# Performance work log

Hardware: AMD Instinct MI355X
Metric: run time of the kernel (lower is better)

Reference implementation:

```python
import jax, jax.numpy as jnp
import numpy as np

N, P = 512, 256
GAMMA = 1.0


def _linear_w(key, out_dim, in_dim):
    # torch nn.Linear default init: U(-1/sqrt(fan_in), 1/sqrt(fan_in))
    bound = 1.0 / np.sqrt(in_dim)
    return jax.random.uniform(key, (out_dim, in_dim), jnp.float32, -bound, bound)


def setup_inputs() -> dict:
    key = jax.random.key(0)
    ks = jax.random.split(key, 11)
    grad = jax.random.normal(ks[0], (N, P), jnp.float32)
    gradm1 = jax.random.normal(ks[1], (N, P), jnp.float32)
    dm1 = jax.random.normal(ks[2], (N, P), jnp.float32)
    # reset_mat(n_traj=N): identity per trajectory
    predicted_mat = jnp.broadcast_to(jnp.eye(P, dtype=jnp.float32), (N, P, P)).copy()
    return {
        "grad": grad, "gradm1": gradm1, "dm1": dm1, "predicted_mat": predicted_mat,
        "W_fullskip": _linear_w(ks[3], 1, 6),
        "Wo1": _linear_w(ks[4], 6, 3),
        "Wo2": _linear_w(ks[5], 12, 6),
        "Wo3": _linear_w(ks[6], 3, 12),
        "Wl1": _linear_w(ks[7], 12, 6),
        "Wl2": _linear_w(ks[8], 24, 12),
        "Wl3": _linear_w(ks[9], 1, 24),
    }


def reference(grad, gradm1, dm1, predicted_mat, W_fullskip, Wo1, Wo2, Wo3, Wl1, Wl2, Wl3):
    relu = jax.nn.relu
    # --- construct_features (torch.no_grad) ---
    QNDG = jnp.einsum('npq,nq->np', predicted_mat, grad - gradm1)          # (N,P)
    Bg = -GAMMA * jnp.einsum('npq,nq->np', predicted_mat, grad)            # (N,P)
    # cat along feature dim then reshape(N,3,P).transpose -> stack on last axis
    x = jnp.stack([QNDG, dm1, Bg], axis=-1)                                # (N,P,3)
    x = jax.lax.stop_gradient(x)
    # --- outer_FF: per-coordinate tiny MLP, then mean over P ---
    of = relu(x @ Wo1.T)
    of = relu(of @ Wo2.T)
    of = of @ Wo3.T                                                        # (N,P,3)
    of = jnp.mean(of, axis=1)                                              # (N,3)
    of = jnp.broadcast_to(of[:, None, :], x.shape)                         # (N,P,3)
    x6 = jnp.concatenate([x, of], axis=-1)                                 # (N,P,6)
    # --- full skip connection ---
    fullskip = (x6 @ W_fullskip.T)[..., 0]                                 # (N,P)
    # --- inner MLP (layers) ---
    out = relu(x6 @ Wl1.T)
    out = relu(out @ Wl2.T)
    out = (out @ Wl3.T)[..., 0]                                            # (N,P)
    out = out + fullskip
    # --- BFGS-like rank-2 update ---
    DGK = grad - gradm1                                                    # (N,P)
    secant = x[:, :, 1] - x[:, :, 0]                                       # dm1 - QNDG
    denom = jnp.sum(out * DGK, axis=-1, keepdims=True)                     # (N,1)
    normalization = (1.0 / denom)[:, :, None]                              # (N,1,1)
    coef = (jnp.sum(secant * DGK, axis=-1, keepdims=True) / denom)[:, :, None]
    upd = normalization * (
        secant[:, :, None] * out[:, None, :]
        + out[:, :, None] * secant[:, None, :]
        - coef * out[:, :, None] * out[:, None, :]
    )                                                                      # (N,P,P)
    new_mat = predicted_mat + upd
    v = -jax.lax.stop_gradient(grad)
    d = jnp.einsum('npq,nq->np', new_mat, v)                               # (N,P)
    return d
```

## Files before the change

### kernel.cpp

```cpp
#include <hip/hip_runtime.h>

#define NT 512
#define PD 256
#define TROWS 32
#define NTILES 8
#define LPITCH 257

__device__ __forceinline__ float wave_reduce_sum(float v) {
    #pragma unroll
    for (int m = 32; m >= 1; m >>= 1) v += __shfl_xor(v, m, 64);
    return v;
}

__global__ __launch_bounds__(256) void fused_kernel(
    const float* __restrict__ pm, const float* __restrict__ grad,
    const float* __restrict__ gradm1, const float* __restrict__ dm1,
    const float* __restrict__ Wfs, const float* __restrict__ Wo1,
    const float* __restrict__ Wo2, const float* __restrict__ Wo3,
    const float* __restrict__ Wl1, const float* __restrict__ Wl2,
    const float* __restrict__ Wl3, float* __restrict__ dout)
{
    __shared__ float buf0[TROWS * LPITCH];
    __shared__ float buf1[TROWS * LPITCH];
    __shared__ float sW[516];
    __shared__ float redA[4][3];
    __shared__ float redB[4][4];

    const int t    = threadIdx.x;
    const int lane = t & 63;
    const int wave = t >> 6;
    const int n    = blockIdx.x;

    if (t < 18) sW[t]       = Wo1[t];
    if (t < 72) sW[18 + t]  = Wo2[t];
    if (t < 36) sW[90 + t]  = Wo3[t];
    if (t < 72) sW[126 + t] = Wl1[t];
    sW[198 + t] = Wl2[t];
    if (t < 32) sW[198 + 256 + t] = Wl2[256 + t];
    if (t < 24) sW[486 + t] = Wl3[t];
    if (t < 6)  sW[510 + t] = Wfs[t];

    const int r  = t & 31;
    const int cg = t >> 5;
    float gv[32], dgv[32];
    {
        const float4* gb  = (const float4*)(grad   + n * PD + cg * 32);
        const float4* gmb = (const float4*)(gradm1 + n * PD + cg * 32);
        #pragma unroll
        for (int i = 0; i < 8; ++i) {
            float4 a = gb[i];
            float4 b = gmb[i];
            gv[4*i+0] = a.x; gv[4*i+1] = a.y; gv[4*i+2] = a.z; gv[4*i+3] = a.w;
            dgv[4*i+0] = a.x - b.x; dgv[4*i+1] = a.y - b.y;
            dgv[4*i+2] = a.z - b.z; dgv[4*i+3] = a.w - b.w;
        }
    }

    const float* tbase = pm + (size_t)n * PD * PD;
    float4 stg[8];
    float accq[NTILES], accg[NTILES];


    #pragma unroll
    for (int j = 0; j < 8; ++j) {
        const int row = 4 * j + wave;
        stg[j] = ((const float4*)(tbase + (size_t)(0 * TROWS + row) * PD))[lane];
    }
    #pragma unroll
    for (int j = 0; j < 8; ++j) {
        const int row = 4 * j + wave;
        float* p = buf0 + row * LPITCH + lane;
        p[0] = stg[j].x; p[64] = stg[j].y; p[128] = stg[j].z; p[192] = stg[j].w;
    }
    __syncthreads();

    #pragma unroll
    for (int k = 0; k < NTILES; ++k) {
        if (k + 1 < NTILES) {
            #pragma unroll
            for (int j = 0; j < 8; ++j) {
                const int row = 4 * j + wave;
                stg[j] = ((const float4*)(tbase + (size_t)((k + 1) * TROWS + row) * PD))[lane];
            }
        }
        {
            const float* bp = ((k & 1) ? buf1 : buf0) + r * LPITCH + 8 * cg;
            float sq = 0.f, sg = 0.f;
            #pragma unroll
            for (int p = 0; p < 4; ++p) {
                #pragma unroll
                for (int q = 0; q < 8; ++q) {
                    const float m = bp[p * 64 + q];
                    sq += m * dgv[4*q + p];
                    sg += m * gv[4*q + p];
                }
            }
            accq[k] = sq; accg[k] = sg;
        }
        if (k + 1 < NTILES) {
            float* wb = ((k + 1) & 1) ? buf1 : buf0;
            #pragma unroll
            for (int j = 0; j < 8; ++j) {
                const int row = 4 * j + wave;
                float* p = wb + row * LPITCH + lane;
                p[0] = stg[j].x; p[64] = stg[j].y; p[128] = stg[j].z; p[192] = stg[j].w;
            }
        }
        __syncthreads();
    }

    float* partsQ = buf0;
    float* partsG = buf0 + 2048;
    #pragma unroll
    for (int k = 0; k < NTILES; ++k) {
        partsQ[k * 256 + t] = accq[k];
        partsG[k * 256 + t] = accg[k];
    }
    __syncthreads();

    float q = 0.f, pg = 0.f;
    {
        const int pb = (t >> 5) * 256 + (t & 31);
        #pragma unroll
        for (int c = 0; c < 8; ++c) {
            q  += partsQ[pb + 32 * c];
            pg += partsG[pb + 32 * c];
        }
    }

    const int idx = n * PD + t;
    const float bg = -pg;
    const float g  = gv[t & 31];
    const float gm = g - dgv[t & 31];
    const float dm = dm1[idx];

    const float x0 = q, x1 = dm, x2 = bg;

    float h1[6];
    #pragma unroll
    for (int j = 0; j < 6; ++j) {
        float s = sW[j*3] * x0 + sW[j*3 + 1] * x1 + sW[j*3 + 2] * x2;
        h1[j] = fmaxf(s, 0.f);
    }
    float h2[12];
    #pragma unroll
    for (int j = 0; j < 12; ++j) {
        float s = 0.f;
        #pragma unroll
        for (int i = 0; i < 6; ++i) s += sW[18 + j*6 + i] * h1[i];
        h2[j] = fmaxf(s, 0.f);
    }
    float o0 = 0.f, o1 = 0.f, o2 = 0.f;
    #pragma unroll
    for (int i = 0; i < 12; ++i) {
        o0 += sW[90 + i]      * h2[i];
        o1 += sW[90 + 12 + i] * h2[i];
        o2 += sW[90 + 24 + i] * h2[i];
    }

    float r0 = wave_reduce_sum(o0);
    float r1 = wave_reduce_sum(o1);
    float r2 = wave_reduce_sum(o2);
    if (lane == 0) { redA[wave][0] = r0; redA[wave][1] = r1; redA[wave][2] = r2; }
    __syncthreads();
    const float inv = 1.0f / 256.0f;
    const float of0 = (redA[0][0] + redA[1][0] + redA[2][0] + redA[3][0]) * inv;
    const float of1 = (redA[0][1] + redA[1][1] + redA[2][1] + redA[3][1]) * inv;
    const float of2 = (redA[0][2] + redA[1][2] + redA[2][2] + redA[3][2]) * inv;

    const float x6[6] = {x0, x1, x2, of0, of1, of2};

    float fullskip = 0.f;
    #pragma unroll
    for (int i = 0; i < 6; ++i) fullskip += sW[510 + i] * x6[i];

    float l1[12];
    #pragma unroll
    for (int j = 0; j < 12; ++j) {
        float s = 0.f;
        #pragma unroll
        for (int i = 0; i < 6; ++i) s += sW[126 + j*6 + i] * x6[i];
        l1[j] = fmaxf(s, 0.f);
    }
    float l2[24];
    #pragma unroll
    for (int j = 0; j < 24; ++j) {
        float s = 0.f;
        #pragma unroll
        for (int i = 0; i < 12; ++i) s += sW[198 + j*12 + i] * l1[i];
        l2[j] = fmaxf(s, 0.f);
    }
    float out = fullskip;
    #pragma unroll
    for (int i = 0; i < 24; ++i) out += sW[486 + i] * l2[i];

    const float dgk    = g - gm;
    const float secant = dm - q;

    float pd  = wave_reduce_sum(out * dgk);
    float ps  = wave_reduce_sum(secant * dgk);
    float po  = wave_reduce_sum(out * g);
    float psg = wave_reduce_sum(secant * g);
    if (lane == 0) {
        redB[wave][0] = pd; redB[wave][1] = ps;
        redB[wave][2] = po; redB[wave][3] = psg;
    }
    __syncthreads();
    const float denom = redB[0][0] + redB[1][0] + redB[2][0] + redB[3][0];
    const float sdgk  = redB[0][1] + redB[1][1] + redB[2][1] + redB[3][1];
    const float og    = redB[0][2] + redB[1][2] + redB[2][2] + redB[3][2];
    const float sg2   = redB[0][3] + redB[1][3] + redB[2][3] + redB[3][3];

    const float invd = 1.0f / denom;
    const float coef = sdgk * invd;
    const float d = bg + (-secant * og - out * sg2 + coef * out * og) * invd;
    dout[idx] = d;
}

extern "C" void kernel_launch(void* const* d_in, const int* in_sizes, int n_in,
                              void* d_out, int out_size, void* d_ws, size_t ws_size,
                              hipStream_t stream) {
    const float* grad   = (const float*)d_in[0];
    const float* gradm1 = (const float*)d_in[1];
    const float* dm1    = (const float*)d_in[2];
    const float* pm     = (const float*)d_in[3];
    const float* Wfs    = (const float*)d_in[4];
    const float* Wo1    = (const float*)d_in[5];
    const float* Wo2    = (const float*)d_in[6];
    const float* Wo3    = (const float*)d_in[7];
    const float* Wl1    = (const float*)d_in[8];
    const float* Wl2    = (const float*)d_in[9];
    const float* Wl3    = (const float*)d_in[10];

    fused_kernel<<<NT, 256, 0, stream>>>(pm, grad, gradm1, dm1,
                                         Wfs, Wo1, Wo2, Wo3, Wl1, Wl2, Wl3,
                                         (float*)d_out);
}
```

Before: 218.2 us.

## Stream matrix rows directly into registers with shuffle reductions instead of LDS tiles

Replaces the double-buffered LDS staging of the 256x256 per-trajectory matrix with direct float4 global loads. Each group of 16 lanes reads one row, and the row dot products against grad and its difference are finished with xor shuffles. A one-iteration register prefetch keeps loads in flight, and the occupancy hint is raised. This removes the LDS transposed writes, the eight block-wide barriers and the partial-sum reduction pass. In exchange it adds per-row shuffle reductions and keeps fewer bytes in flight per thread.

Result: no change. 217.6 us (-0.3%).

```diff
diff --git a/kernel.cpp b/kernel.cpp
--- a/kernel.cpp
+++ b/kernel.cpp
@@ -2,9 +2,6 @@
 
 #define NT 512
 #define PD 256
-#define TROWS 32
-#define NTILES 8
-#define LPITCH 257
 
 __device__ __forceinline__ float wave_reduce_sum(float v) {
     #pragma unroll
@@ -12,7 +9,7 @@
     return v;
 }
 
-__global__ __launch_bounds__(256) void fused_kernel(
+__global__ __launch_bounds__(256, 4) void fused_kernel(
     const float* __restrict__ pm, const float* __restrict__ grad,
     const float* __restrict__ gradm1, const float* __restrict__ dm1,
     const float* __restrict__ Wfs, const float* __restrict__ Wo1,
@@ -20,8 +17,10 @@
     const float* __restrict__ Wl1, const float* __restrict__ Wl2,
     const float* __restrict__ Wl3, float* __restrict__ dout)
 {
-    __shared__ float buf0[TROWS * LPITCH];
-    __shared__ float buf1[TROWS * LPITCH];
+    __shared__ __align__(16) float sdg[PD];
+    __shared__ __align__(16) float sgv[PD];
+    __shared__ float qres[PD];
+    __shared__ float pgres[PD];
     __shared__ float sW[516];
     __shared__ float redA[4][3];
     __shared__ float redB[4][4];
@@ -30,6 +29,8 @@
     const int lane = t & 63;
     const int wave = t >> 6;
     const int n    = blockIdx.x;
+    const int l15  = lane & 15;
+    const int l4   = lane >> 4;
 
     if (t < 18) sW[t]       = Wo1[t];
     if (t < 72) sW[18 + t]  = Wo2[t];
@@ -40,99 +41,64 @@
     if (t < 24) sW[486 + t] = Wl3[t];
     if (t < 6)  sW[510 + t] = Wfs[t];
 
-    const int r  = t & 31;
-    const int cg = t >> 5;
-    float gv[32], dgv[32];
-    {
-        const float4* gb  = (const float4*)(grad   + n * PD + cg * 32);
-        const float4* gmb = (const float4*)(gradm1 + n * PD + cg * 32);
-        #pragma unroll
-        for (int i = 0; i < 8; ++i) {
-            float4 a = gb[i];
-            float4 b = gmb[i];
-            gv[4*i+0] = a.x; gv[4*i+1] = a.y; gv[4*i+2] = a.z; gv[4*i+3] = a.w;
-            dgv[4*i+0] = a.x - b.x; dgv[4*i+1] = a.y - b.y;
-            dgv[4*i+2] = a.z - b.z; dgv[4*i+3] = a.w - b.w;
-        }
-    }
-
-    const float* tbase = pm + (size_t)n * PD * PD;
-    float4 stg[8];
-    float accq[NTILES], accg[NTILES];
-
-
-    #pragma unroll
-    for (int j = 0; j < 8; ++j) {
-        const int row = 4 * j + wave;
-        stg[j] = ((const float4*)(tbase + (size_t)(0 * TROWS + row) * PD))[lane];
-    }
-    #pragma unroll
-    for (int j = 0; j < 8; ++j) {
-        const int row = 4 * j + wave;
-        float* p = buf0 + row * LPITCH + lane;
-        p[0] = stg[j].x; p[64] = stg[j].y; p[128] = stg[j].z; p[192] = stg[j].w;
-    }
-    __syncthreads();
-
-    #pragma unroll
-    for (int k = 0; k < NTILES; ++k) {
-        if (k + 1 < NTILES) {
+    const int idx = n * PD + t;
+    const float g_t  = grad[idx];
+    const float gm_t = gradm1[idx];
+    const float dm_t = dm1[idx];
+    sdg[t] = g_t - gm_t;
+    sgv[t] = g_t;
+    __syncthreads();
+
+    float dgv[16], gvv[16];
+    #pragma unroll
+    for (int j = 0; j < 4; ++j) {
+        const float4 a = ((const float4*)(sdg + 64 * j))[l15];
+        const float4 b = ((const float4*)(sgv + 64 * j))[l15];
+        dgv[4*j+0] = a.x; dgv[4*j+1] = a.y; dgv[4*j+2] = a.z; dgv[4*j+3] = a.w;
+        gvv[4*j+0] = b.x; gvv[4*j+1] = b.y; gvv[4*j+2] = b.z; gvv[4*j+3] = b.w;
+    }
+
+    const float* rb = pm + (size_t)n * PD * PD
+                    + (size_t)(64 * wave + l4) * PD + 4 * l15;
+
+    float4 cur[4], nxt[4];
+    #pragma unroll
+    for (int j = 0; j < 4; ++j) cur[j] = *(const float4*)(rb + 64 * j);
+
+    #pragma unroll 1
+    for (int it = 0; it < 16; ++it) {
+        if (it < 15) {
+            const float* rb2 = rb + (size_t)(it + 1) * 4 * PD;
             #pragma unroll
-            for (int j = 0; j < 8; ++j) {
-                const int row = 4 * j + wave;
-                stg[j] = ((const float4*)(tbase + (size_t)((k + 1) * TROWS + row) * PD))[lane];
-            }
-        }
-        {
-            const float* bp = ((k & 1) ? buf1 : buf0) + r * LPITCH + 8 * cg;
-            float sq = 0.f, sg = 0.f;
-            #pragma unroll
-            for (int p = 0; p < 4; ++p) {
-                #pragma unroll
-                for (int q = 0; q < 8; ++q) {
-                    const float m = bp[p * 64 + q];
-                    sq += m * dgv[4*q + p];
-                    sg += m * gv[4*q + p];
-                }
-            }
-            accq[k] = sq; accg[k] = sg;
-        }
-        if (k + 1 < NTILES) {
-            float* wb = ((k + 1) & 1) ? buf1 : buf0;
-            #pragma unroll
-            for (int j = 0; j < 8; ++j) {
-                const int row = 4 * j + wave;
-                float* p = wb + row * LPITCH + lane;
-                p[0] = stg[j].x; p[64] = stg[j].y; p[128] = stg[j].z; p[192] = stg[j].w;
-            }
-        }
-        __syncthreads();
-    }
-
-    float* partsQ = buf0;
-    float* partsG = buf0 + 2048;
-    #pragma unroll
-    for (int k = 0; k < NTILES; ++k) {
-        partsQ[k * 256 + t] = accq[k];
-        partsG[k * 256 + t] = accg[k];
-    }
-    __syncthreads();
-
-    float q = 0.f, pg = 0.f;
-    {
-        const int pb = (t >> 5) * 256 + (t & 31);
-        #pragma unroll
-        for (int c = 0; c < 8; ++c) {
-            q  += partsQ[pb + 32 * c];
-            pg += partsG[pb + 32 * c];
-        }
-    }
-
-    const int idx = n * PD + t;
+            for (int j = 0; j < 4; ++j) nxt[j] = *(const float4*)(rb2 + 64 * j);
+        }
+        float sq = 0.f, sg = 0.f;
+        #pragma unroll
+        for (int j = 0; j < 4; ++j) {
+            sq += cur[j].x * dgv[4*j+0]; sg += cur[j].x * gvv[4*j+0];
+            sq += cur[j].y * dgv[4*j+1]; sg += cur[j].y * gvv[4*j+1];
+            sq += cur[j].z * dgv[4*j+2]; sg += cur[j].z * gvv[4*j+2];
+            sq += cur[j].w * dgv[4*j+3]; sg += cur[j].w * gvv[4*j+3];
+        }
+        #pragma unroll
+        for (int m = 1; m <= 8; m <<= 1) {
+            sq += __shfl_xor(sq, m, 64);
+            sg += __shfl_xor(sg, m, 64);
+        }
+        if (l15 == 0) {
+            const int row = 64 * wave + 4 * it + l4;
+            qres[row]  = sq;
+            pgres[row] = sg;
+        }
+        #pragma unroll
+        for (int j = 0; j < 4; ++j) cur[j] = nxt[j];
+    }
+    __syncthreads();
+
+    const float q  = qres[t];
+    const float pg = pgres[t];
     const float bg = -pg;
-    const float g  = gv[t & 31];
-    const float gm = g - dgv[t & 31];
-    const float dm = dm1[idx];
+    const float dm = dm_t;
 
     const float x0 = q, x1 = dm, x2 = bg;
 
@@ -194,13 +160,13 @@
     #pragma unroll
     for (int i = 0; i < 24; ++i) out += sW[486 + i] * l2[i];
 
-    const float dgk    = g - gm;
+    const float dgk    = g_t - gm_t;
     const float secant = dm - q;
 
     float pd  = wave_reduce_sum(out * dgk);
     float ps  = wave_reduce_sum(secant * dgk);
-    float po  = wave_reduce_sum(out * g);
-    float psg = wave_reduce_sum(secant * g);
+    float po  = wave_reduce_sum(out * g_t);
+    float psg = wave_reduce_sum(secant * g_t);
     if (lane == 0) {
         redB[wave][0] = pd; redB[wave][1] = ps;
         redB[wave][2] = po; redB[wave][3] = psg;
```
